# Kernel optimization log

Measured on AMD Instinct MI355X. Metric: run time of the kernel, lower is better.

## Reference

```python
import jax, jax.numpy as jnp
import numpy as np

B, S, HID = 2, 2048, 2304
H, KVH, D = 8, 4, 256          # query heads, kv heads, head_dim
N_REP = H // KVH
SCALE = 256.0 ** -0.5          # query_pre_attn_scalar ** -0.5
SOFTCAP = 50.0
ROPE_THETA = 10000.0
NEG = -1e9


def setup_inputs() -> dict:
    key = jax.random.key(0)
    k1, k2, k3, k4, k5 = jax.random.split(key, 5)
    hidden_states = jax.random.normal(k1, (B, S, HID), dtype=jnp.float32)
    # RoPE cos/sin tables, shape [B, S, D]
    inv_freq = 1.0 / (ROPE_THETA ** (jnp.arange(0, D, 2, dtype=jnp.float32) / D))
    pos = jnp.arange(S, dtype=jnp.float32)
    freqs = pos[:, None] * inv_freq[None, :]            # [S, D/2]
    emb = jnp.concatenate([freqs, freqs], axis=-1)      # [S, D]
    cos = jnp.broadcast_to(jnp.cos(emb)[None], (B, S, D))
    sin = jnp.broadcast_to(jnp.sin(emb)[None], (B, S, D))
    # additive causal mask [B, 1, S, S] (sliding_window=4096 > S, so pure causal)
    idx = jnp.arange(S)
    causal = idx[None, :] <= idx[:, None]
    attention_mask = jnp.broadcast_to(
        jnp.where(causal, 0.0, NEG).astype(jnp.float32)[None, None], (B, 1, S, S))
    # projection weights (lecun-normal-ish scale), no bias (attention_bias=False)
    Wq = jax.random.normal(k2, (HID, H * D), dtype=jnp.float32) / np.sqrt(HID)
    Wk = jax.random.normal(k3, (HID, KVH * D), dtype=jnp.float32) / np.sqrt(HID)
    Wv = jax.random.normal(k4, (HID, KVH * D), dtype=jnp.float32) / np.sqrt(HID)
    Wo = jax.random.normal(k5, (H * D, HID), dtype=jnp.float32) / np.sqrt(H * D)
    return {"hidden_states": hidden_states, "cos": cos, "sin": sin,
            "attention_mask": attention_mask,
            "Wq": Wq, "Wk": Wk, "Wv": Wv, "Wo": Wo}


def _rotate_half(x):
    half = x.shape[-1] // 2
    return jnp.concatenate([-x[..., half:], x[..., :half]], axis=-1)


def reference(hidden_states, cos, sin, attention_mask, Wq, Wk, Wv, Wo):
    b, s, _ = hidden_states.shape
    q = (hidden_states @ Wq).reshape(b, s, H, D).transpose(0, 2, 1, 3)    # [B,H,S,D]
    k = (hidden_states @ Wk).reshape(b, s, KVH, D).transpose(0, 2, 1, 3)  # [B,KVH,S,D]
    v = (hidden_states @ Wv).reshape(b, s, KVH, D).transpose(0, 2, 1, 3)
    c = cos[:, None]  # [B,1,S,D] broadcast over heads (unsqueeze_dim=1)
    sn = sin[:, None]
    q = q * c + _rotate_half(q) * sn
    k = k * c + _rotate_half(k) * sn
    # GQA: repeat kv heads (interleave, matching repeat_kv tile+reshape)
    k = jnp.repeat(k, N_REP, axis=1)
    v = jnp.repeat(v, N_REP, axis=1)
    w = jnp.einsum('bhqd,bhkd->bhqk', q, k) * SCALE
    w = jnp.tanh(w / SOFTCAP) * SOFTCAP                  # logit softcapping
    w = w + attention_mask[:, :, :, :s]
    w = jax.nn.softmax(w.astype(jnp.float32), axis=-1).astype(q.dtype)
    out = jnp.einsum('bhqk,bhkd->bhqd', w, v)
    out = out.transpose(0, 2, 1, 3).reshape(b, s, H * D)
    return out @ Wo
```

## Files before the change

kernel.cpp:

```cpp
#include <hip/hip_runtime.h>

typedef unsigned short u16;
typedef __attribute__((ext_vector_type(8))) short short8;
typedef __attribute__((ext_vector_type(4))) float f32x4;

constexpr int B_ = 2;
constexpr int H_ = 8;
constexpr int KVH_ = 4;
constexpr int S_ = 2048;
constexpr int D_ = 256;
constexpr int HID_ = 2304;
constexpr int QKVN_ = 4096;
constexpr int AON_ = 2048;

__device__ __forceinline__ float b2f(u16 u) {
  union { float f; unsigned int i; } x; x.i = ((unsigned int)u) << 16; return x.f;
}
__device__ __forceinline__ u16 f2b(float f) {
  unsigned int x = __float_as_uint(f);
  unsigned int r = (x + 0x7fffu + ((x >> 16) & 1u)) >> 16;
  return (u16)r;
}

__global__ void cast_kernel(const float* __restrict__ in, u16* __restrict__ out) {
  size_t i = ((size_t)blockIdx.x * 256 + threadIdx.x) * 4;
  float4 v = *(const float4*)(in + i);
  unsigned int lo = (unsigned int)f2b(v.x) | ((unsigned int)f2b(v.y) << 16);
  unsigned int hi = (unsigned int)f2b(v.z) | ((unsigned int)f2b(v.w) << 16);
  uint2 o; o.x = lo; o.y = hi;
  *(uint2*)(out + i) = o;
}

__global__ void transpose_cast_all(const float* __restrict__ s0, const float* __restrict__ s1,
                                   const float* __restrict__ s2, const float* __restrict__ s3,
                                   u16* __restrict__ d0, u16* __restrict__ d1,
                                   u16* __restrict__ d2, u16* __restrict__ d3) {
  __shared__ float tile[64][65];
  int which = blockIdx.z;
  const float* src; u16* dst; int R, C;
  if (which == 0)      { src = s0; dst = d0; R = 2304; C = 2048; }
  else if (which == 1) { src = s1; dst = d1; R = 2304; C = 1024; }
  else if (which == 2) { src = s2; dst = d2; R = 2304; C = 1024; }
  else                 { src = s3; dst = d3; R = 2048; C = 2304; }
  int r0 = blockIdx.y * 64, c0 = blockIdx.x * 64;
  if (r0 >= R || c0 >= C) return;
  int t = threadIdx.x;
#pragma unroll
  for (int i = 0; i < 16; ++i) {
    int e = i * 256 + t;
    int r = e >> 6, c = e & 63;
    tile[r][c] = src[(size_t)(r0 + r) * C + (c0 + c)];
  }
  __syncthreads();
#pragma unroll
  for (int i = 0; i < 16; ++i) {
    int e = i * 256 + t;
    int orow = e >> 6, ocol = e & 63;
    dst[(size_t)(c0 + orow) * R + (r0 + ocol)] = f2b(tile[ocol][orow]);
  }
}

template <int OUTF32>
__global__ __launch_bounds__(512, 2) void gemm_bt8(
    const u16* __restrict__ A, const u16* __restrict__ B, void* __restrict__ Cp,
    int M, int N, int K) {
  __shared__ u16 lds[2][2][2][8192];
  const int tid = threadIdx.x;
  const int lane = tid & 63;
  const int wave = tid >> 6;
  const int wm = wave >> 2, wn = wave & 3;
  const int quad = lane >> 4, l16 = lane & 15;
  const int m0 = blockIdx.y * 256, n0 = blockIdx.x * 256;
  const int nt = K >> 6;

  const int sub = tid >> 6;
  const int rr = (tid >> 2) & 15;
  const int cc = ((tid & 3) * 8) ^ ((rr & 8) ? 16 : 0);
  const int r_rel = (sub >> 1) * 16 + rr;
  const int ccol = (sub & 1) * 32 + cc;
  const u16* Asrc = A + (size_t)(m0 + r_rel) * K + ccol;
  const u16* Bsrc = B + (size_t)(n0 + r_rel) * K + ccol;
  const int ldsc = tid * 8;

  const int fr_off = l16 * 64 + (((quad * 8) ^ ((l16 & 8) ? 16 : 0)) << 1);

#define GL8(src, dst)                                                                  \
  __builtin_amdgcn_global_load_lds((const __attribute__((address_space(1))) void*)(src), \
                                   (__attribute__((address_space(3))) void*)(dst), 16, 0, 0)
#define STAGE_A(bf, kt, qp) {                                                          \
    const u16* _s = Asrc + (size_t)(kt) * 64;                                          \
    GL8(_s + (size_t)((qp) * 64) * K,       &lds[bf][0][0][(qp) * 4096 + ldsc]);       \
    GL8(_s + (size_t)(128 + (qp) * 64) * K, &lds[bf][0][1][(qp) * 4096 + ldsc]); }
#define STAGE_B(bf, kt, hf) {                                                          \
    const u16* _s = Bsrc + (size_t)(kt) * 64;                                          \
    GL8(_s + (size_t)((hf) * 128) * K,      &lds[bf][1][hf][ldsc]);                    \
    GL8(_s + (size_t)((hf) * 128 + 64) * K, &lds[bf][1][hf][4096 + ldsc]); }
#define LDA(bf, mi, kk) \
  (*(const short8*)((const char*)&lds[bf][0][wm][0] + (mi) * 2048 + (kk) * 1024 + fr_off))
#define LDB(bf, ni, kk) \
  (*(const short8*)((const char*)&lds[bf][1][wn >> 1][0] + ((wn & 1) * 4 + (ni)) * 2048 + (kk) * 1024 + fr_off))

  f32x4 acc[8][4] = {};
  short8 bfr[4][2], af[2][2];

  STAGE_B(0, 0, 0); STAGE_B(0, 0, 1); STAGE_A(0, 0, 0); STAGE_A(0, 0, 1);
  STAGE_B(1, 1, 0); STAGE_B(1, 1, 1); STAGE_A(1, 1, 0);
  asm volatile("s_waitcnt vmcnt(6)" ::: "memory");
  __builtin_amdgcn_s_barrier();

#define PHASE(q, STG, VMW)                                                             \
    _Pragma("unroll") for (int i = 0; i < 2; ++i)                                      \
      _Pragma("unroll") for (int kk = 0; kk < 2; ++kk) af[i][kk] = LDA(c, 2 * (q) + i, kk); \
    STG; VMW;                                                                          \
    __builtin_amdgcn_s_barrier();                                                      \
    asm volatile("s_waitcnt lgkmcnt(0)" ::: "memory");                                 \
    __builtin_amdgcn_sched_barrier(0);                                                 \
    __builtin_amdgcn_s_setprio(1);                                                     \
    _Pragma("unroll") for (int i = 0; i < 2; ++i)                                      \
      _Pragma("unroll") for (int ni = 0; ni < 4; ++ni)                                 \
        _Pragma("unroll") for (int kk = 0; kk < 2; ++kk)                               \
          acc[2 * (q) + i][ni] = __builtin_amdgcn_mfma_f32_16x16x32_bf16(              \
              af[i][kk], bfr[ni][kk], acc[2 * (q) + i][ni], 0, 0, 0);                  \
    __builtin_amdgcn_s_setprio(0);                                                     \
    __builtin_amdgcn_s_barrier();

  for (int T = 0; T < nt; ++T) {
    const int c = T & 1;
#pragma unroll
    for (int ni = 0; ni < 4; ++ni)
#pragma unroll
      for (int kk = 0; kk < 2; ++kk) bfr[ni][kk] = LDB(c, ni, kk);
    PHASE(0, if (T + 1 < nt) STAGE_A(c ^ 1, T + 1, 1), )
    PHASE(1, if (T + 2 < nt) STAGE_B(c, T + 2, 0), )
    PHASE(2, if (T + 2 < nt) STAGE_B(c, T + 2, 1), )
    PHASE(3, if (T + 2 < nt) STAGE_A(c, T + 2, 0),
          if (T + 2 >= nt) { asm volatile("s_waitcnt vmcnt(0)" ::: "memory"); }
          else             { asm volatile("s_waitcnt vmcnt(6)" ::: "memory"); })
  }
#undef PHASE
#undef LDA
#undef LDB
#undef STAGE_A
#undef STAGE_B
#undef GL8

#pragma unroll
  for (int mi = 0; mi < 8; ++mi) {
#pragma unroll
    for (int ni = 0; ni < 4; ++ni) {
#pragma unroll
      for (int r = 0; r < 4; ++r) {
        int row = m0 + wm * 128 + mi * 16 + quad * 4 + r;
        int col = n0 + wn * 64 + ni * 16 + l16;
        if (OUTF32)
          ((float*)Cp)[(size_t)row * N + col] = acc[mi][ni][r];
        else
          ((u16*)Cp)[(size_t)row * N + col] = f2b(acc[mi][ni][r]);
      }
    }
  }
}

__global__ void rope_kernel(const u16* __restrict__ qkv, const float* __restrict__ cs,
                            const float* __restrict__ sn, u16* __restrict__ Qr,
                            u16* __restrict__ Kr) {
  int row = blockIdx.x;
  int b = row >> 11, s = row & 2047;
  int d = threadIdx.x;
  const u16* qrow = qkv + (size_t)row * QKVN_;
  float c = cs[(size_t)row * D_ + d];
  float si = sn[(size_t)row * D_ + d];
  int dp = (d < 128) ? d + 128 : d - 128;
  float sgn = (d < 128) ? -1.f : 1.f;
#pragma unroll
  for (int h = 0; h < H_; ++h) {
    float v = b2f(qrow[h * D_ + d]);
    float p = sgn * b2f(qrow[h * D_ + dp]);
    Qr[((size_t)(b * H_ + h) * S_ + s) * D_ + d] = f2b(v * c + p * si);
  }
#pragma unroll
  for (int g = 0; g < KVH_; ++g) {
    float v = b2f(qrow[2048 + g * D_ + d]);
    float p = sgn * b2f(qrow[2048 + g * D_ + dp]);
    Kr[((size_t)(b * KVH_ + g) * S_ + s) * D_ + d] = f2b(v * c + p * si);
  }
}

__global__ void transpose_v(const u16* __restrict__ qkv, u16* __restrict__ Vt) {
  __shared__ u16 tile[64][72];
  int d0 = blockIdx.x * 64, s0 = blockIdx.y * 64, g = blockIdx.z;
  int b = g >> 2, kvh = g & 3;
  int t = threadIdx.x;
#pragma unroll
  for (int i = 0; i < 16; ++i) {
    int e = i * 256 + t;
    int r = e >> 6, c = e & 63;
    tile[r][c] = qkv[(size_t)(b * S_ + s0 + r) * QKVN_ + 3072 + kvh * D_ + d0 + c];
  }
  __syncthreads();
#pragma unroll
  for (int i = 0; i < 16; ++i) {
    int e = i * 256 + t;
    int orow = e >> 6, ocol = e & 63;
    Vt[((size_t)g * D_ + d0 + orow) * S_ + s0 + ocol] = tile[ocol][orow];
  }
}

__global__ __launch_bounds__(256, 1) void attn_kernel(
    const u16* __restrict__ Qr, const u16* __restrict__ Kr, const u16* __restrict__ Vt,
    float* __restrict__ Op0, float* __restrict__ Op1,
    float* __restrict__ Lp0, float* __restrict__ Lp1) {
  __shared__ u16 Ks[2][32 * 256];
  __shared__ u16 Vs[2][32 * 256];
  int u = blockIdx.x >> 1, sp = blockIdx.x & 1;
  int h = blockIdx.y;
  int kvh = h >> 1;
  int tid = threadIdx.x, wave = tid >> 6, lane = tid & 63;
  int quad = lane >> 4, l16 = lane & 15;
  float* Op = sp ? Op1 : Op0;
  float* Lp = sp ? Lp1 : Lp0;
  const int kst_r = tid >> 5;
  const int kst_c = (tid & 31) ^ ((tid >> 5) & 3);
  const int vst_r = tid >> 2;
  const int vst_c = (tid & 3) ^ ((tid >> 3) & 3);
  const int kg = l16 >> 2, ka = l16 & 3;
  const int srow0 = 8 * kg + ka;
  const int ksw = ka | ((kg & 1) << 2);

  for (int part = 0; part < 2; ++part) {
    int b = part;
    int qt = (part == 0) ? u : (15 - u);
    int q0 = qt * 128;
    int beg = sp ? (2 * qt + 2) : 0;
    int end = sp ? (4 * qt + 4) : (2 * qt + 2);
    const u16* Qbase = Qr + ((size_t)(b * H_ + h) * S_ + q0 + wave * 32 + l16) * D_;
    short8 qf[2][8];
#pragma unroll
    for (int f = 0; f < 2; ++f)
#pragma unroll
      for (int kk = 0; kk < 8; ++kk)
        qf[f][kk] = *(const short8*)(Qbase + (size_t)f * 16 * D_ + kk * 32 + quad * 8);
    const u16* Kbase = Kr + (size_t)(b * KVH_ + kvh) * S_ * D_;
    const u16* Vbase = Vt + (size_t)(b * KVH_ + kvh) * D_ * S_;
    float lp[2] = {0.f, 0.f};
    f32x4 o_acc[2][16] = {};
    const int qq0 = q0 + wave * 32 + l16;

#define STAGE(KT, BUF)                                                                   \
    {                                                                                    \
      int k0s = (KT) * 32;                                                               \
      _Pragma("unroll") for (int i = 0; i < 4; ++i) {                                    \
        int p = i * 256 + tid;                                                           \
        __builtin_amdgcn_global_load_lds(                                                \
            (const __attribute__((address_space(1))) void*)(Kbase +                      \
                (size_t)(k0s + i * 8 + kst_r) * D_ + (kst_c ^ ((i & 1) << 2)) * 8),      \
            (__attribute__((address_space(3))) void*)(&Ks[BUF][0] + p * 8), 16, 0, 0);   \
      }                                                                                  \
      _Pragma("unroll") for (int i = 0; i < 4; ++i) {                                    \
        int p = i * 256 + tid;                                                           \
        __builtin_amdgcn_global_load_lds(                                                \
            (const __attribute__((address_space(1))) void*)(Vbase +                      \
                (size_t)(i * 64 + vst_r) * S_ + k0s + vst_c * 8),                        \
            (__attribute__((address_space(3))) void*)(&Vs[BUF][0] + p * 8), 16, 0, 0);   \
      }                                                                                  \
    }

    STAGE(beg, 0);
    __syncthreads();
    for (int kt = beg; kt < end; ++kt) {
      int k0 = kt * 32;
      int cur = (kt - beg) & 1;
      if (kt + 1 < end) STAGE(kt + 1, cur ^ 1);
      f32x4 sacc[2][2] = {};
      __builtin_amdgcn_s_setprio(1);
#pragma unroll
      for (int n = 0; n < 2; ++n) {
        const u16* kb = &Ks[cur][0] + (srow0 + 4 * n) * 256;
#pragma unroll
        for (int kk = 0; kk < 8; ++kk) {
          int phys = (kk * 4 + quad) ^ ksw;
          short8 kfr = *(const short8*)(kb + phys * 8);
          sacc[0][n] = __builtin_amdgcn_mfma_f32_16x16x32_bf16(kfr, qf[0][kk], sacc[0][n], 0, 0, 0);
          sacc[1][n] = __builtin_amdgcn_mfma_f32_16x16x32_bf16(kfr, qf[1][kk], sacc[1][n], 0, 0, 0);
        }
      }
      __builtin_amdgcn_s_setprio(0);
      bool full = (k0 + 31 <= q0 + wave * 32);
      short8 pa[2];
#pragma unroll
      for (int f = 0; f < 2; ++f) {
        union { short8 s8; unsigned int d[4]; } pu;
#pragma unroll
        for (int n = 0; n < 2; ++n) {
#pragma unroll
          for (int r = 0; r < 4; ++r) {
            float E = __expf(sacc[f][n][r] * 0.0025f);
            float ee = __expf(-100.0f * __frcp_rn(E + 1.0f));
            if (!full) {
              int key = k0 + 8 * quad + 4 * n + r;
              ee = (key <= qq0 + f * 16) ? ee : 0.0f;
            }
            lp[f] += ee;
            sacc[f][n][r] = ee;
          }
          pu.d[2 * n]     = (unsigned int)f2b(sacc[f][n][0]) | ((unsigned int)f2b(sacc[f][n][1]) << 16);
          pu.d[2 * n + 1] = (unsigned int)f2b(sacc[f][n][2]) | ((unsigned int)f2b(sacc[f][n][3]) << 16);
        }
        pa[f] = pu.s8;
      }
      __builtin_amdgcn_s_setprio(1);
#pragma unroll
      for (int dt = 0; dt < 16; ++dt) {
        int d = dt * 16 + l16;
        int phys = quad ^ ((d >> 1) & 3);
        short8 vb = *(const short8*)(&Vs[cur][0] + d * 32 + phys * 8);
        o_acc[0][dt] = __builtin_amdgcn_mfma_f32_16x16x32_bf16(pa[0], vb, o_acc[0][dt], 0, 0, 0);
        o_acc[1][dt] = __builtin_amdgcn_mfma_f32_16x16x32_bf16(pa[1], vb, o_acc[1][dt], 0, 0, 0);
      }
      __builtin_amdgcn_s_setprio(0);
      __syncthreads();
    }
#undef STAGE
#pragma unroll
    for (int f = 0; f < 2; ++f) {
      lp[f] += __shfl_xor(lp[f], 16, 64);
      lp[f] += __shfl_xor(lp[f], 32, 64);
    }
    if (lane < 16) {
      size_t lb = ((size_t)(b * H_ + h)) * S_ + q0 + wave * 32 + lane;
      Lp[lb] = lp[0];
      Lp[lb + 16] = lp[1];
    }
#pragma unroll
    for (int f = 0; f < 2; ++f)
#pragma unroll
      for (int dt = 0; dt < 16; ++dt)
#pragma unroll
        for (int r = 0; r < 4; ++r) {
          int row = b * S_ + q0 + wave * 32 + f * 16 + quad * 4 + r;
          int col = h * D_ + dt * 16 + l16;
          Op[(size_t)row * AON_ + col] = o_acc[f][dt][r];
        }
  }
}

__global__ void combine_kernel(const float* __restrict__ Op0, const float* __restrict__ Op1,
                               const float* __restrict__ Lp0, const float* __restrict__ Lp1,
                               u16* __restrict__ Ao) {
  size_t idx = (size_t)blockIdx.x * 256 + threadIdx.x;
  size_t row = idx >> 9;
  int c4 = ((int)idx & 511) * 4;
  const float4 a = *(const float4*)(Op0 + row * AON_ + c4);
  const float4 b4 = *(const float4*)(Op1 + row * AON_ + c4);
  int b = (int)(row >> 11), s = (int)row & 2047;
  int h = c4 >> 8;
  size_t li = ((size_t)(b * H_ + h)) * S_ + s;
  float inv = 1.0f / (Lp0[li] + Lp1[li]);
  unsigned int lo = (unsigned int)f2b((a.x + b4.x) * inv) | ((unsigned int)f2b((a.y + b4.y) * inv) << 16);
  unsigned int hi = (unsigned int)f2b((a.z + b4.z) * inv) | ((unsigned int)f2b((a.w + b4.w) * inv) << 16);
  uint2 o; o.x = lo; o.y = hi;
  *(uint2*)(Ao + row * AON_ + c4) = o;
}

extern "C" void kernel_launch(void* const* d_in, const int* in_sizes, int n_in,
                              void* d_out, int out_size, void* d_ws, size_t ws_size,
                              hipStream_t stream) {
  const float* hidden = (const float*)d_in[0];
  const float* cosp = (const float*)d_in[1];
  const float* sinp = (const float*)d_in[2];
  const float* Wq = (const float*)d_in[4];
  const float* Wk = (const float*)d_in[5];
  const float* Wv = (const float*)d_in[6];
  const float* Wo = (const float*)d_in[7];

  u16* hs  = (u16*)d_ws;
  u16* WT  = hs  + (size_t)4096 * HID_;
  u16* WoT = WT  + (size_t)4096 * HID_;
  u16* qkv = WoT + (size_t)HID_ * AON_;
  u16* Qr  = qkv + (size_t)4096 * QKVN_;
  u16* Kr  = Qr  + (size_t)B_ * H_ * S_ * D_;
  u16* Vt  = Kr  + (size_t)B_ * KVH_ * S_ * D_;
  u16* Ao  = Vt  + (size_t)B_ * KVH_ * S_ * D_;
  float* Lp0 = (float*)(Ao + (size_t)4096 * AON_);
  float* Lp1 = Lp0 + (size_t)B_ * H_ * S_;
  float* Op0 = (float*)hs;
  float* Op1 = (float*)qkv;

  cast_kernel<<<9216, 256, 0, stream>>>(hidden, hs);
  transpose_cast_all<<<dim3(36, 36, 4), 256, 0, stream>>>(
      Wq, Wk, Wv, Wo, WT, WT + (size_t)2048 * HID_, WT + (size_t)3072 * HID_, WoT);
  gemm_bt8<0><<<dim3(16, 16), 512, 0, stream>>>(hs, WT, qkv, 4096, QKVN_, HID_);
  rope_kernel<<<4096, 256, 0, stream>>>(qkv, cosp, sinp, Qr, Kr);
  transpose_v<<<dim3(4, 32, 8), 256, 0, stream>>>(qkv, Vt);
  attn_kernel<<<dim3(32, 8), 256, 0, stream>>>(Qr, Kr, Vt, Op0, Op1, Lp0, Lp1);
  combine_kernel<<<16384, 256, 0, stream>>>(Op0, Op1, Lp0, Lp1, Ao);
  gemm_bt8<1><<<dim3(9, 16), 512, 0, stream>>>(Ao, WoT, d_out, 4096, HID_, 2048);
}
```

Baseline: 433.4 us.

## Split attention blocks per batch and allow two blocks per CU

Turns the attention grid from 256 blocks, each looping over both batches, into 512 single-batch blocks. A flat index maps to batch, head, split half and a query tile, with tiles ordered so heavy and light causal tiles interleave. Launch bounds go from 1 to 2 blocks per CU so more blocks can be resident and latency hidden better, at the cost of tighter register limits. With the large o_acc array, that tighter register budget risks spilling.

```diff
diff --git a/kernel.cpp b/kernel.cpp
--- a/kernel.cpp
+++ b/kernel.cpp
@@ -206,14 +206,21 @@
   }
 }
 
-__global__ __launch_bounds__(256, 1) void attn_kernel(
+__global__ __launch_bounds__(256, 2) void attn_kernel(
     const u16* __restrict__ Qr, const u16* __restrict__ Kr, const u16* __restrict__ Vt,
     float* __restrict__ Op0, float* __restrict__ Op1,
     float* __restrict__ Lp0, float* __restrict__ Lp1) {
   __shared__ u16 Ks[2][32 * 256];
   __shared__ u16 Vs[2][32 * 256];
-  int u = blockIdx.x >> 1, sp = blockIdx.x & 1;
-  int h = blockIdx.y;
+  int bx = blockIdx.x;
+  int b = bx >> 8;
+  int r = bx & 255;
+  int h = r >> 5;
+  int rem = r & 31;
+  int sp = rem >> 4;
+  int t = rem & 15;
+  int qt0 = (t & 1) ? (15 - (t >> 1)) : (t >> 1);
+  int qt = b ? (15 - qt0) : qt0;
   int kvh = h >> 1;
   int tid = threadIdx.x, wave = tid >> 6, lane = tid & 63;
   int quad = lane >> 4, l16 = lane & 15;
@@ -227,121 +234,117 @@
   const int srow0 = 8 * kg + ka;
   const int ksw = ka | ((kg & 1) << 2);
 
-  for (int part = 0; part < 2; ++part) {
-    int b = part;
-    int qt = (part == 0) ? u : (15 - u);
-    int q0 = qt * 128;
-    int beg = sp ? (2 * qt + 2) : 0;
-    int end = sp ? (4 * qt + 4) : (2 * qt + 2);
-    const u16* Qbase = Qr + ((size_t)(b * H_ + h) * S_ + q0 + wave * 32 + l16) * D_;
-    short8 qf[2][8];
-#pragma unroll
-    for (int f = 0; f < 2; ++f)
-#pragma unroll
-      for (int kk = 0; kk < 8; ++kk)
-        qf[f][kk] = *(const short8*)(Qbase + (size_t)f * 16 * D_ + kk * 32 + quad * 8);
-    const u16* Kbase = Kr + (size_t)(b * KVH_ + kvh) * S_ * D_;
-    const u16* Vbase = Vt + (size_t)(b * KVH_ + kvh) * D_ * S_;
-    float lp[2] = {0.f, 0.f};
-    f32x4 o_acc[2][16] = {};
-    const int qq0 = q0 + wave * 32 + l16;
-
-#define STAGE(KT, BUF)                                                                   \
-    {                                                                                    \
-      int k0s = (KT) * 32;                                                               \
-      _Pragma("unroll") for (int i = 0; i < 4; ++i) {                                    \
-        int p = i * 256 + tid;                                                           \
-        __builtin_amdgcn_global_load_lds(                                                \
-            (const __attribute__((address_space(1))) void*)(Kbase +                      \
-                (size_t)(k0s + i * 8 + kst_r) * D_ + (kst_c ^ ((i & 1) << 2)) * 8),      \
-            (__attribute__((address_space(3))) void*)(&Ks[BUF][0] + p * 8), 16, 0, 0);   \
-      }                                                                                  \
-      _Pragma("unroll") for (int i = 0; i < 4; ++i) {                                    \
-        int p = i * 256 + tid;                                                           \
-        __builtin_amdgcn_global_load_lds(                                                \
-            (const __attribute__((address_space(1))) void*)(Vbase +                      \
-                (size_t)(i * 64 + vst_r) * S_ + k0s + vst_c * 8),                        \
-            (__attribute__((address_space(3))) void*)(&Vs[BUF][0] + p * 8), 16, 0, 0);   \
-      }                                                                                  \
+  int q0 = qt * 128;
+  int beg = sp ? (2 * qt + 2) : 0;
+  int end = sp ? (4 * qt + 4) : (2 * qt + 2);
+  const u16* Qbase = Qr + ((size_t)(b * H_ + h) * S_ + q0 + wave * 32 + l16) * D_;
+  short8 qf[2][8];
+#pragma unroll
+  for (int f = 0; f < 2; ++f)
+#pragma unroll
+    for (int kk = 0; kk < 8; ++kk)
+      qf[f][kk] = *(const short8*)(Qbase + (size_t)f * 16 * D_ + kk * 32 + quad * 8);
+  const u16* Kbase = Kr + (size_t)(b * KVH_ + kvh) * S_ * D_;
+  const u16* Vbase = Vt + (size_t)(b * KVH_ + kvh) * D_ * S_;
+  float lp[2] = {0.f, 0.f};
+  f32x4 o_acc[2][16] = {};
+  const int qq0 = q0 + wave * 32 + l16;
+
+#define STAGE(KT, BUF)                                                                 \
+  {                                                                                    \
+    int k0s = (KT) * 32;                                                               \
+    _Pragma("unroll") for (int i = 0; i < 4; ++i) {                                    \
+      int p = i * 256 + tid;                                                           \
+      __builtin_amdgcn_global_load_lds(                                                \
+          (const __attribute__((address_space(1))) void*)(Kbase +                      \
+              (size_t)(k0s + i * 8 + kst_r) * D_ + (kst_c ^ ((i & 1) << 2)) * 8),      \
+          (__attribute__((address_space(3))) void*)(&Ks[BUF][0] + p * 8), 16, 0, 0);   \
+    }                                                                                  \
+    _Pragma("unroll") for (int i = 0; i < 4; ++i) {                                    \
+      int p = i * 256 + tid;                                                           \
+      __builtin_amdgcn_global_load_lds(                                                \
+          (const __attribute__((address_space(1))) void*)(Vbase +                      \
+              (size_t)(i * 64 + vst_r) * S_ + k0s + vst_c * 8),                        \
+          (__attribute__((address_space(3))) void*)(&Vs[BUF][0] + p * 8), 16, 0, 0);   \
+    }                                                                                  \
+  }
+
+  STAGE(beg, 0);
+  __syncthreads();
+  for (int kt = beg; kt < end; ++kt) {
+    int k0 = kt * 32;
+    int cur = (kt - beg) & 1;
+    if (kt + 1 < end) STAGE(kt + 1, cur ^ 1);
+    f32x4 sacc[2][2] = {};
+    __builtin_amdgcn_s_setprio(1);
+#pragma unroll
+    for (int n = 0; n < 2; ++n) {
+      const u16* kb = &Ks[cur][0] + (srow0 + 4 * n) * 256;
+#pragma unroll
+      for (int kk = 0; kk < 8; ++kk) {
+        int phys = (kk * 4 + quad) ^ ksw;
+        short8 kfr = *(const short8*)(kb + phys * 8);
+        sacc[0][n] = __builtin_amdgcn_mfma_f32_16x16x32_bf16(kfr, qf[0][kk], sacc[0][n], 0, 0, 0);
+        sacc[1][n] = __builtin_amdgcn_mfma_f32_16x16x32_bf16(kfr, qf[1][kk], sacc[1][n], 0, 0, 0);
+      }
     }
-
-    STAGE(beg, 0);
+    __builtin_amdgcn_s_setprio(0);
+    bool full = (k0 + 31 <= q0 + wave * 32);
+    short8 pa[2];
+#pragma unroll
+    for (int f = 0; f < 2; ++f) {
+      union { short8 s8; unsigned int d[4]; } pu;
+#pragma unroll
+      for (int n = 0; n < 2; ++n) {
+#pragma unroll
+        for (int rr2 = 0; rr2 < 4; ++rr2) {
+          float E = __expf(sacc[f][n][rr2] * 0.0025f);
+          float ee = __expf(-100.0f * __frcp_rn(E + 1.0f));
+          if (!full) {
+            int key = k0 + 8 * quad + 4 * n + rr2;
+            ee = (key <= qq0 + f * 16) ? ee : 0.0f;
+          }
+          lp[f] += ee;
+          sacc[f][n][rr2] = ee;
+        }
+        pu.d[2 * n]     = (unsigned int)f2b(sacc[f][n][0]) | ((unsigned int)f2b(sacc[f][n][1]) << 16);
+        pu.d[2 * n + 1] = (unsigned int)f2b(sacc[f][n][2]) | ((unsigned int)f2b(sacc[f][n][3]) << 16);
+      }
+      pa[f] = pu.s8;
+    }
+    __builtin_amdgcn_s_setprio(1);
+#pragma unroll
+    for (int dt = 0; dt < 16; ++dt) {
+      int d = dt * 16 + l16;
+      int phys = quad ^ ((d >> 1) & 3);
+      short8 vb = *(const short8*)(&Vs[cur][0] + d * 32 + phys * 8);
+      o_acc[0][dt] = __builtin_amdgcn_mfma_f32_16x16x32_bf16(pa[0], vb, o_acc[0][dt], 0, 0, 0);
+      o_acc[1][dt] = __builtin_amdgcn_mfma_f32_16x16x32_bf16(pa[1], vb, o_acc[1][dt], 0, 0, 0);
+    }
+    __builtin_amdgcn_s_setprio(0);
     __syncthreads();
-    for (int kt = beg; kt < end; ++kt) {
-      int k0 = kt * 32;
-      int cur = (kt - beg) & 1;
-      if (kt + 1 < end) STAGE(kt + 1, cur ^ 1);
-      f32x4 sacc[2][2] = {};
-      __builtin_amdgcn_s_setprio(1);
-#pragma unroll
-      for (int n = 0; n < 2; ++n) {
-        const u16* kb = &Ks[cur][0] + (srow0 + 4 * n) * 256;
-#pragma unroll
-        for (int kk = 0; kk < 8; ++kk) {
-          int phys = (kk * 4 + quad) ^ ksw;
-          short8 kfr = *(const short8*)(kb + phys * 8);
-          sacc[0][n] = __builtin_amdgcn_mfma_f32_16x16x32_bf16(kfr, qf[0][kk], sacc[0][n], 0, 0, 0);
-          sacc[1][n] = __builtin_amdgcn_mfma_f32_16x16x32_bf16(kfr, qf[1][kk], sacc[1][n], 0, 0, 0);
-        }
+  }
+#undef STAGE
+#pragma unroll
+  for (int f = 0; f < 2; ++f) {
+    lp[f] += __shfl_xor(lp[f], 16, 64);
+    lp[f] += __shfl_xor(lp[f], 32, 64);
+  }
+  if (lane < 16) {
+    size_t lb = ((size_t)(b * H_ + h)) * S_ + q0 + wave * 32 + lane;
+    Lp[lb] = lp[0];
+    Lp[lb + 16] = lp[1];
+  }
+#pragma unroll
+  for (int f = 0; f < 2; ++f)
+#pragma unroll
+    for (int dt = 0; dt < 16; ++dt)
+#pragma unroll
+      for (int rr2 = 0; rr2 < 4; ++rr2) {
+        int row = b * S_ + q0 + wave * 32 + f * 16 + quad * 4 + rr2;
+        int col = h * D_ + dt * 16 + l16;
+        Op[(size_t)row * AON_ + col] = o_acc[f][dt][rr2];
       }
-      __builtin_amdgcn_s_setprio(0);
-      bool full = (k0 + 31 <= q0 + wave * 32);
-      short8 pa[2];
-#pragma unroll
-      for (int f = 0; f < 2; ++f) {
-        union { short8 s8; unsigned int d[4]; } pu;
-#pragma unroll
-        for (int n = 0; n < 2; ++n) {
-#pragma unroll
-          for (int r = 0; r < 4; ++r) {
-            float E = __expf(sacc[f][n][r] * 0.0025f);
-            float ee = __expf(-100.0f * __frcp_rn(E + 1.0f));
-            if (!full) {
-              int key = k0 + 8 * quad + 4 * n + r;
-              ee = (key <= qq0 + f * 16) ? ee : 0.0f;
-            }
-            lp[f] += ee;
-            sacc[f][n][r] = ee;
-          }
-          pu.d[2 * n]     = (unsigned int)f2b(sacc[f][n][0]) | ((unsigned int)f2b(sacc[f][n][1]) << 16);
-          pu.d[2 * n + 1] = (unsigned int)f2b(sacc[f][n][2]) | ((unsigned int)f2b(sacc[f][n][3]) << 16);
-        }
-        pa[f] = pu.s8;
-      }
-      __builtin_amdgcn_s_setprio(1);
-#pragma unroll
-      for (int dt = 0; dt < 16; ++dt) {
-        int d = dt * 16 + l16;
-        int phys = quad ^ ((d >> 1) & 3);
-        short8 vb = *(const short8*)(&Vs[cur][0] + d * 32 + phys * 8);
-        o_acc[0][dt] = __builtin_amdgcn_mfma_f32_16x16x32_bf16(pa[0], vb, o_acc[0][dt], 0, 0, 0);
-        o_acc[1][dt] = __builtin_amdgcn_mfma_f32_16x16x32_bf16(pa[1], vb, o_acc[1][dt], 0, 0, 0);
-      }
-      __builtin_amdgcn_s_setprio(0);
-      __syncthreads();
-    }
-#undef STAGE
-#pragma unroll
-    for (int f = 0; f < 2; ++f) {
-      lp[f] += __shfl_xor(lp[f], 16, 64);
-      lp[f] += __shfl_xor(lp[f], 32, 64);
-    }
-    if (lane < 16) {
-      size_t lb = ((size_t)(b * H_ + h)) * S_ + q0 + wave * 32 + lane;
-      Lp[lb] = lp[0];
-      Lp[lb + 16] = lp[1];
-    }
-#pragma unroll
-    for (int f = 0; f < 2; ++f)
-#pragma unroll
-      for (int dt = 0; dt < 16; ++dt)
-#pragma unroll
-        for (int r = 0; r < 4; ++r) {
-          int row = b * S_ + q0 + wave * 32 + f * 16 + quad * 4 + r;
-          int col = h * D_ + dt * 16 + l16;
-          Op[(size_t)row * AON_ + col] = o_acc[f][dt][r];
-        }
-  }
 }
 
 __global__ void combine_kernel(const float* __restrict__ Op0, const float* __restrict__ Op1,
@@ -392,7 +395,7 @@
   gemm_bt8<0><<<dim3(16, 16), 512, 0, stream>>>(hs, WT, qkv, 4096, QKVN_, HID_);
   rope_kernel<<<4096, 256, 0, stream>>>(qkv, cosp, sinp, Qr, Kr);
   transpose_v<<<dim3(4, 32, 8), 256, 0, stream>>>(qkv, Vt);
-  attn_kernel<<<dim3(32, 8), 256, 0, stream>>>(Qr, Kr, Vt, Op0, Op1, Lp0, Lp1);
+  attn_kernel<<<dim3(512), 256, 0, stream>>>(Qr, Kr, Vt, Op0, Op1, Lp0, Lp1);
   combine_kernel<<<16384, 256, 0, stream>>>(Op0, Op1, Lp0, Lp1, Ao);
   gemm_bt8<1><<<dim3(9, 16), 512, 0, stream>>>(Ao, WoT, d_out, 4096, HID_, 2048);
 }
```

Measured after the change: 424.3 us. -2.1%, faster.
